# Kernel tuning notes

Measured on AMD Instinct MI355X. Metric: run time of the kernel, lower is better.

## Reference

```python
import jax, jax.numpy as jnp
import numpy as np

N_NODES = 100000
N_EDGES = 3200000
D = 16
L = 3


def setup_inputs() -> dict:
    key = jax.random.key(0)
    ks = jax.random.split(key, 7)
    scale = 1.0 / np.sqrt(D)
    x = jax.random.normal(ks[0], (N_NODES, D), dtype=jnp.float32)
    edge_index = jax.random.randint(ks[1], (2, N_EDGES), 0, N_NODES, dtype=jnp.int64)
    Wl = jax.random.normal(ks[2], (L, D, D), dtype=jnp.float32) * scale
    bl = jax.random.normal(ks[3], (L, D), dtype=jnp.float32) * scale
    Wr = jax.random.normal(ks[4], (L, D, D), dtype=jnp.float32) * scale
    Wlin = jax.random.normal(ks[5], (L, D, D), dtype=jnp.float32) * scale
    blin = jax.random.normal(ks[6], (L, D), dtype=jnp.float32) * scale
    return {"x": x, "edge_index": edge_index, "Wl": Wl, "bl": bl,
            "Wr": Wr, "Wlin": Wlin, "blin": blin}


def reference(x, edge_index, Wl, bl, Wr, Wlin, blin):
    src = edge_index[0]
    dst = edge_index[1]
    n = x.shape[0]
    # in-degree for mean aggregation (PyG SAGEConv aggr='mean')
    deg = jax.ops.segment_sum(jnp.ones((src.shape[0],), dtype=x.dtype), dst,
                              num_segments=n)
    denom = jnp.maximum(deg, 1.0)[:, None]  # nodes with no in-edges -> 0 agg
    for i in range(Wl.shape[0]):
        # gather source features, scatter-mean onto targets
        agg = jax.ops.segment_sum(x[src], dst, num_segments=n) / denom
        conv = agg @ Wl[i].T + bl[i] + x @ Wr[i].T  # SAGEConv: lin_l(agg)+lin_r(x)
        x = conv + x @ Wlin[i].T + blin[i]          # + Linear residual
    return x
```

## Files before the change

kernel.cpp:

```cpp
#include <hip/hip_runtime.h>

#define N_NODES 100000
#define N_EDGES 3200000
#define D 16
#define L 3

#define TILE 64
#define NB ((N_NODES + TILE - 1) / TILE)
#define CAP 3072
#define NBLK 500
#define SEG (N_EDGES / NBLK)
#define BINT 1024

__device__ __forceinline__ unsigned packbf(float a, float b) {
    unsigned ua = __float_as_uint(a); ua += 0x7FFFu + ((ua >> 16) & 1u);
    unsigned ub = __float_as_uint(b); ub += 0x7FFFu + ((ub >> 16) & 1u);
    return (ua >> 16) | (ub & 0xFFFF0000u);
}
#define BLO(u) __uint_as_float((u) << 16)
#define BHI(u) __uint_as_float((u) & 0xFFFF0000u)

__global__ void cvt_kernel(const float* __restrict__ x, unsigned* __restrict__ xbf, int n4) {
    int t = blockIdx.x * blockDim.x + threadIdx.x;
    if (t >= n4) return;
    float4 v = *(const float4*)(x + (size_t)t * 4);
    uint2 o; o.x = packbf(v.x, v.y); o.y = packbf(v.z, v.w);
    *(uint2*)(xbf + (size_t)t * 2) = o;
}

__global__ void bin_scatter(const int* __restrict__ src, const int* __restrict__ dst,
                            int* __restrict__ cursor, unsigned* __restrict__ ebuf, int E) {
    __shared__ int lcnt[NB];
    __shared__ int lbase[NB];
    for (int i = threadIdx.x; i < NB; i += BINT) lcnt[i] = 0;
    __syncthreads();
    int b0 = blockIdx.x * SEG, b1 = min(E, b0 + SEG);
    for (int e = b0 + threadIdx.x * 4; e < b1; e += BINT * 4) {
        int4 d4 = *(const int4*)(dst + e);
        atomicAdd(&lcnt[d4.x >> 6], 1);
        atomicAdd(&lcnt[d4.y >> 6], 1);
        atomicAdd(&lcnt[d4.z >> 6], 1);
        atomicAdd(&lcnt[d4.w >> 6], 1);
    }
    __syncthreads();
    for (int i = threadIdx.x; i < NB; i += BINT) {
        int v = lcnt[i];
        lbase[i] = v ? (i * CAP + atomicAdd(&cursor[i], v)) : 0;
    }
    __syncthreads();
    for (int i = threadIdx.x; i < NB; i += BINT) lcnt[i] = 0;
    __syncthreads();
    for (int e = b0 + threadIdx.x * 4; e < b1; e += BINT * 4) {
        int4 d4 = *(const int4*)(dst + e);
        int4 s4 = *(const int4*)(src + e);
        int b_, pos;
        b_ = d4.x >> 6; pos = lbase[b_] + atomicAdd(&lcnt[b_], 1);
        ebuf[pos] = ((unsigned)(d4.x & 63) << 17) | (unsigned)s4.x;
        b_ = d4.y >> 6; pos = lbase[b_] + atomicAdd(&lcnt[b_], 1);
        ebuf[pos] = ((unsigned)(d4.y & 63) << 17) | (unsigned)s4.y;
        b_ = d4.z >> 6; pos = lbase[b_] + atomicAdd(&lcnt[b_], 1);
        ebuf[pos] = ((unsigned)(d4.z & 63) << 17) | (unsigned)s4.z;
        b_ = d4.w >> 6; pos = lbase[b_] + atomicAdd(&lcnt[b_], 1);
        ebuf[pos] = ((unsigned)(d4.w & 63) << 17) | (unsigned)s4.w;
    }
}

__device__ __forceinline__ void agg_xform(
    const float* __restrict__ xin, const unsigned* __restrict__ xbf,
    const unsigned* se2, const int* lofs,
    const float* sWl, const float* sWc, const float* sbc,
    float* __restrict__ xout, unsigned* __restrict__ xbf_out,
    int emit_bf, int b, int N, int tid) {
    int n_loc = tid >> 2;
    int q = tid & 3;
    int n = b * TILE + n_loc;
    if (n >= N) return;

    int s0 = lofs[n_loc];
    int s1 = lofs[n_loc + 1];
    int deg = s1 - s0;

    float a0 = 0.f, a1 = 0.f, a2 = 0.f, a3 = 0.f;
    float c0 = 0.f, c1 = 0.f, c2 = 0.f, c3 = 0.f;
    int i = s0;
    for (; i + 8 <= s1; i += 8) {
        uint2 g[8];
        #pragma unroll
        for (int j = 0; j < 8; j++) {
            unsigned p = se2[i + j] & 0x1FFFF;
            g[j] = *(const uint2*)(xbf + (size_t)p * 8 + q * 2);
        }
        #pragma unroll
        for (int j = 0; j < 8; j += 2) {
            a0 += BLO(g[j].x); a1 += BHI(g[j].x); a2 += BLO(g[j].y); a3 += BHI(g[j].y);
            c0 += BLO(g[j + 1].x); c1 += BHI(g[j + 1].x); c2 += BLO(g[j + 1].y); c3 += BHI(g[j + 1].y);
        }
    }
    for (; i < s1; i++) {
        unsigned p = se2[i] & 0x1FFFF;
        uint2 g = *(const uint2*)(xbf + (size_t)p * 8 + q * 2);
        a0 += BLO(g.x); a1 += BHI(g.x); a2 += BLO(g.y); a3 += BHI(g.y);
    }
    a0 += c0; a1 += c1; a2 += c2; a3 += c3;

    float inv = 1.0f / fmaxf((float)deg, 1.0f);
    float a[4] = { a0 * inv, a1 * inv, a2 * inv, a3 * inv };
    float4 xq = *(const float4*)(xin + (size_t)n * D + q * 4);
    float xv[4] = { xq.x, xq.y, xq.z, xq.w };

    float o[4];
    #pragma unroll
    for (int j = 0; j < D; j++) {
        float p = 0.f;
        #pragma unroll
        for (int k = 0; k < 4; k++) {
            int kk = q * 4 + k;
            p += a[k] * sWl[j * D + kk] + xv[k] * sWc[j * D + kk];
        }
        p += __shfl_xor(p, 1, 4);
        p += __shfl_xor(p, 2, 4);
        if ((j >> 2) == q) o[j & 3] = p + sbc[j];
    }
    *(float4*)(xout + (size_t)n * D + q * 4) = make_float4(o[0], o[1], o[2], o[3]);
    if (emit_bf) {
        uint2 ob; ob.x = packbf(o[0], o[1]); ob.y = packbf(o[2], o[3]);
        *(uint2*)(xbf_out + (size_t)n * 8 + q * 2) = ob;
    }
}

__global__ void layer0_kernel(const float* __restrict__ xin, const unsigned* __restrict__ xbf,
                              unsigned* __restrict__ ebuf, const int* __restrict__ cnt,
                              int* __restrict__ node_start,
                              const float* __restrict__ Wl, const float* __restrict__ bl,
                              const float* __restrict__ Wr, const float* __restrict__ Wlin,
                              const float* __restrict__ blin,
                              float* __restrict__ xout, unsigned* __restrict__ xbf_out, int N) {
    __shared__ unsigned se[CAP];
    __shared__ unsigned se2[CAP];
    __shared__ int lcnt[TILE];
    __shared__ int lofs[TILE + 1];
    __shared__ float sWl[D * D];
    __shared__ float sWc[D * D];
    __shared__ float sbc[D];

    int tid = threadIdx.x;
    int b = blockIdx.x;
    int base = b * CAP;
    int nE = min(cnt[b], CAP);

    if (tid < D * D) { sWl[tid] = Wl[tid]; sWc[tid] = Wr[tid] + Wlin[tid]; }
    if (tid < D) sbc[tid] = bl[tid] + blin[tid];
    if (tid < TILE) lcnt[tid] = 0;
    __syncthreads();
    for (int i = tid; i < nE; i += 256) {
        unsigned p = ebuf[base + i];
        se[i] = p;
        atomicAdd(&lcnt[p >> 17], 1);
    }
    __syncthreads();
    if (tid < TILE) {
        int v = lcnt[tid];
        int s = v;
        #pragma unroll
        for (int d_ = 1; d_ < TILE; d_ <<= 1) {
            int t = __shfl_up(s, d_, TILE);
            if (tid >= d_) s += t;
        }
        int excl = s - v;
        lofs[tid] = excl;
        lcnt[tid] = excl;
        node_start[b * TILE + tid] = excl;
        if (tid == TILE - 1) lofs[TILE] = s;
    }
    __syncthreads();
    for (int i = tid; i < nE; i += 256) {
        unsigned p = se[i];
        int pos = atomicAdd(&lcnt[p >> 17], 1);
        se2[pos] = p;
    }
    __syncthreads();
    for (int i = tid; i < nE; i += 256)
        ebuf[base + i] = se2[i];

    agg_xform(xin, xbf, se2, lofs, sWl, sWc, sbc, xout, xbf_out, 1, b, N, tid);
}

__global__ void layerN_kernel(const float* __restrict__ xin, const unsigned* __restrict__ xbf,
                              const unsigned* __restrict__ ebuf, const int* __restrict__ cnt,
                              const int* __restrict__ node_start,
                              const float* __restrict__ Wl, const float* __restrict__ bl,
                              const float* __restrict__ Wr, const float* __restrict__ Wlin,
                              const float* __restrict__ blin,
                              float* __restrict__ xout, unsigned* __restrict__ xbf_out,
                              int emit_bf, int N) {
    __shared__ unsigned se2[CAP];
    __shared__ int lofs[TILE + 1];
    __shared__ float sWl[D * D];
    __shared__ float sWc[D * D];
    __shared__ float sbc[D];

    int tid = threadIdx.x;
    int b = blockIdx.x;
    int base = b * CAP;
    int nE = min(cnt[b], CAP);

    if (tid < D * D) { sWl[tid] = Wl[tid]; sWc[tid] = Wr[tid] + Wlin[tid]; }
    if (tid < D) sbc[tid] = bl[tid] + blin[tid];
    if (tid < TILE) lofs[tid] = node_start[b * TILE + tid];
    if (tid == 0) lofs[TILE] = nE;
    for (int i = tid; i < nE; i += 256) se2[i] = ebuf[base + i];
    __syncthreads();

    agg_xform(xin, xbf, se2, lofs, sWl, sWc, sbc, xout, xbf_out, emit_bf, b, N, tid);
}

extern "C" void kernel_launch(void* const* d_in, const int* in_sizes, int n_in,
                              void* d_out, int out_size, void* d_ws, size_t ws_size,
                              hipStream_t stream) {
    const float* x    = (const float*)d_in[0];
    const int*   ei   = (const int*)d_in[1];
    const float* Wl   = (const float*)d_in[2];
    const float* bl   = (const float*)d_in[3];
    const float* Wr   = (const float*)d_in[4];
    const float* Wlin = (const float*)d_in[5];
    const float* blin = (const float*)d_in[6];
    float* out = (float*)d_out;

    const int* src = ei;
    const int* dst = ei + N_EDGES;

    char* w = (char*)d_ws;
    unsigned* ebuf   = (unsigned*)w;  w += (size_t)NB * CAP * 4;
    float* bufA      = (float*)w;     w += (size_t)N_NODES * D * 4;
    float* bufB      = (float*)w;     w += (size_t)N_NODES * D * 4;
    unsigned* xbf0   = (unsigned*)w;  w += (size_t)N_NODES * 8 * 4;
    unsigned* xbf1   = (unsigned*)w;  w += (size_t)N_NODES * 8 * 4;
    int*   cursor    = (int*)w;       w += (size_t)NB * 4;
    int*   node_start= (int*)w;       w += (size_t)NB * TILE * 4;

    hipMemsetAsync(cursor, 0, (size_t)NB * 4, stream);
    cvt_kernel<<<(N_NODES * D / 4 + 255) / 256, 256, 0, stream>>>(x, xbf0, N_NODES * D / 4);
    bin_scatter<<<NBLK, BINT, 0, stream>>>(src, dst, cursor, ebuf, N_EDGES);

    layer0_kernel<<<NB, 256, 0, stream>>>(
        x, xbf0, ebuf, cursor, node_start,
        Wl, bl, Wr, Wlin, blin, bufA, xbf1, N_NODES);
    layerN_kernel<<<NB, 256, 0, stream>>>(
        bufA, xbf1, ebuf, cursor, node_start,
        Wl + D * D, bl + D, Wr + D * D, Wlin + D * D, blin + D, bufB, xbf0, 1, N_NODES);
    layerN_kernel<<<NB, 256, 0, stream>>>(
        bufB, xbf0, ebuf, cursor, node_start,
        Wl + 2 * D * D, bl + 2 * D, Wr + 2 * D * D, Wlin + 2 * D * D, blin + 2 * D,
        out, xbf1, 0, N_NODES);
}
```

Baseline: 217.1 us.

## Double node tile and sort nodes by degree within each tile

Doubles the per-block node tile to 128 nodes (512 threads, larger edge capacity) and computes a per-tile permutation that orders nodes by descending in-degree. The permutation is saved to global memory and reused by later layers, so the four lanes of a node and neighbouring nodes in a wavefront have similar edge counts. This targets load imbalance and divergence inside wavefronts during the gather loop. The cost is an O(TILE^2) rank computation in layer 0, a multi-step shared-memory scan with many barriers, and more shared memory per block, which can lower occupancy.

Measured after the change: 215.8 us. Within noise of the previous version (-0.6%).

```diff
diff --git a/kernel.cpp b/kernel.cpp
--- a/kernel.cpp
+++ b/kernel.cpp
@@ -5,12 +5,13 @@
 #define D 16
 #define L 3
 
-#define TILE 64
+#define TILE 128
 #define NB ((N_NODES + TILE - 1) / TILE)
-#define CAP 3072
+#define CAP 4608
 #define NBLK 500
 #define SEG (N_EDGES / NBLK)
 #define BINT 1024
+#define LT 512
 
 __device__ __forceinline__ unsigned packbf(float a, float b) {
     unsigned ua = __float_as_uint(a); ua += 0x7FFFu + ((ua >> 16) & 1u);
@@ -37,10 +38,10 @@
     int b0 = blockIdx.x * SEG, b1 = min(E, b0 + SEG);
     for (int e = b0 + threadIdx.x * 4; e < b1; e += BINT * 4) {
         int4 d4 = *(const int4*)(dst + e);
-        atomicAdd(&lcnt[d4.x >> 6], 1);
-        atomicAdd(&lcnt[d4.y >> 6], 1);
-        atomicAdd(&lcnt[d4.z >> 6], 1);
-        atomicAdd(&lcnt[d4.w >> 6], 1);
+        atomicAdd(&lcnt[d4.x >> 7], 1);
+        atomicAdd(&lcnt[d4.y >> 7], 1);
+        atomicAdd(&lcnt[d4.z >> 7], 1);
+        atomicAdd(&lcnt[d4.w >> 7], 1);
     }
     __syncthreads();
     for (int i = threadIdx.x; i < NB; i += BINT) {
@@ -54,25 +55,23 @@
         int4 d4 = *(const int4*)(dst + e);
         int4 s4 = *(const int4*)(src + e);
         int b_, pos;
-        b_ = d4.x >> 6; pos = lbase[b_] + atomicAdd(&lcnt[b_], 1);
-        ebuf[pos] = ((unsigned)(d4.x & 63) << 17) | (unsigned)s4.x;
-        b_ = d4.y >> 6; pos = lbase[b_] + atomicAdd(&lcnt[b_], 1);
-        ebuf[pos] = ((unsigned)(d4.y & 63) << 17) | (unsigned)s4.y;
-        b_ = d4.z >> 6; pos = lbase[b_] + atomicAdd(&lcnt[b_], 1);
-        ebuf[pos] = ((unsigned)(d4.z & 63) << 17) | (unsigned)s4.z;
-        b_ = d4.w >> 6; pos = lbase[b_] + atomicAdd(&lcnt[b_], 1);
-        ebuf[pos] = ((unsigned)(d4.w & 63) << 17) | (unsigned)s4.w;
+        b_ = d4.x >> 7; pos = lbase[b_] + atomicAdd(&lcnt[b_], 1);
+        ebuf[pos] = ((unsigned)(d4.x & 127) << 17) | (unsigned)s4.x;
+        b_ = d4.y >> 7; pos = lbase[b_] + atomicAdd(&lcnt[b_], 1);
+        ebuf[pos] = ((unsigned)(d4.y & 127) << 17) | (unsigned)s4.y;
+        b_ = d4.z >> 7; pos = lbase[b_] + atomicAdd(&lcnt[b_], 1);
+        ebuf[pos] = ((unsigned)(d4.z & 127) << 17) | (unsigned)s4.z;
+        b_ = d4.w >> 7; pos = lbase[b_] + atomicAdd(&lcnt[b_], 1);
+        ebuf[pos] = ((unsigned)(d4.w & 127) << 17) | (unsigned)s4.w;
     }
 }
 
 __device__ __forceinline__ void agg_xform(
     const float* __restrict__ xin, const unsigned* __restrict__ xbf,
-    const unsigned* se2, const int* lofs,
+    const unsigned* se2, const int* lofs, int n_loc,
     const float* sWl, const float* sWc, const float* sbc,
     float* __restrict__ xout, unsigned* __restrict__ xbf_out,
-    int emit_bf, int b, int N, int tid) {
-    int n_loc = tid >> 2;
-    int q = tid & 3;
+    int emit_bf, int b, int N, int q) {
     int n = b * TILE + n_loc;
     if (n >= N) return;
 
@@ -130,7 +129,7 @@
 
 __global__ void layer0_kernel(const float* __restrict__ xin, const unsigned* __restrict__ xbf,
                               unsigned* __restrict__ ebuf, const int* __restrict__ cnt,
-                              int* __restrict__ node_start,
+                              int* __restrict__ node_start, int* __restrict__ gperm,
                               const float* __restrict__ Wl, const float* __restrict__ bl,
                               const float* __restrict__ Wr, const float* __restrict__ Wlin,
                               const float* __restrict__ blin,
@@ -138,7 +137,10 @@
     __shared__ unsigned se[CAP];
     __shared__ unsigned se2[CAP];
     __shared__ int lcnt[TILE];
+    __shared__ int sscan[TILE];
     __shared__ int lofs[TILE + 1];
+    __shared__ int sdeg[TILE];
+    __shared__ int perm[TILE];
     __shared__ float sWl[D * D];
     __shared__ float sWc[D * D];
     __shared__ float sbc[D];
@@ -152,42 +154,55 @@
     if (tid < D) sbc[tid] = bl[tid] + blin[tid];
     if (tid < TILE) lcnt[tid] = 0;
     __syncthreads();
-    for (int i = tid; i < nE; i += 256) {
+    for (int i = tid; i < nE; i += LT) {
         unsigned p = ebuf[base + i];
         se[i] = p;
         atomicAdd(&lcnt[p >> 17], 1);
     }
     __syncthreads();
+    if (tid < TILE) sscan[tid] = lcnt[tid];
+    __syncthreads();
+    for (int off = 1; off < TILE; off <<= 1) {
+        int t = (tid < TILE && tid >= off) ? sscan[tid - off] : 0;
+        __syncthreads();
+        if (tid < TILE) sscan[tid] += t;
+        __syncthreads();
+    }
     if (tid < TILE) {
-        int v = lcnt[tid];
-        int s = v;
-        #pragma unroll
-        for (int d_ = 1; d_ < TILE; d_ <<= 1) {
-            int t = __shfl_up(s, d_, TILE);
-            if (tid >= d_) s += t;
-        }
-        int excl = s - v;
+        int excl = sscan[tid] - lcnt[tid];
         lofs[tid] = excl;
         lcnt[tid] = excl;
+        sdeg[tid] = sscan[tid] - excl;
         node_start[b * TILE + tid] = excl;
-        if (tid == TILE - 1) lofs[TILE] = s;
-    }
-    __syncthreads();
-    for (int i = tid; i < nE; i += 256) {
+        if (tid == TILE - 1) lofs[TILE] = sscan[tid];
+    }
+    __syncthreads();
+    if (tid < TILE) {
+        int dm = sdeg[tid];
+        int r = 0;
+        for (int j = 0; j < TILE; j++) {
+            int dj = sdeg[j];
+            r += (dj > dm) || (dj == dm && j < tid);
+        }
+        perm[r] = tid;
+        gperm[b * TILE + r] = tid;
+    }
+    for (int i = tid; i < nE; i += LT) {
         unsigned p = se[i];
         int pos = atomicAdd(&lcnt[p >> 17], 1);
         se2[pos] = p;
     }
     __syncthreads();
-    for (int i = tid; i < nE; i += 256)
+    for (int i = tid; i < nE; i += LT)
         ebuf[base + i] = se2[i];
 
-    agg_xform(xin, xbf, se2, lofs, sWl, sWc, sbc, xout, xbf_out, 1, b, N, tid);
+    agg_xform(xin, xbf, se2, lofs, perm[tid >> 2], sWl, sWc, sbc,
+              xout, xbf_out, 1, b, N, tid & 3);
 }
 
 __global__ void layerN_kernel(const float* __restrict__ xin, const unsigned* __restrict__ xbf,
                               const unsigned* __restrict__ ebuf, const int* __restrict__ cnt,
-                              const int* __restrict__ node_start,
+                              const int* __restrict__ node_start, const int* __restrict__ gperm,
                               const float* __restrict__ Wl, const float* __restrict__ bl,
                               const float* __restrict__ Wr, const float* __restrict__ Wlin,
                               const float* __restrict__ blin,
@@ -208,10 +223,12 @@
     if (tid < D) sbc[tid] = bl[tid] + blin[tid];
     if (tid < TILE) lofs[tid] = node_start[b * TILE + tid];
     if (tid == 0) lofs[TILE] = nE;
-    for (int i = tid; i < nE; i += 256) se2[i] = ebuf[base + i];
-    __syncthreads();
-
-    agg_xform(xin, xbf, se2, lofs, sWl, sWc, sbc, xout, xbf_out, emit_bf, b, N, tid);
+    for (int i = tid; i < nE; i += LT) se2[i] = ebuf[base + i];
+    int n_loc = gperm[b * TILE + (tid >> 2)];
+    __syncthreads();
+
+    agg_xform(xin, xbf, se2, lofs, n_loc, sWl, sWc, sbc,
+              xout, xbf_out, emit_bf, b, N, tid & 3);
 }
 
 extern "C" void kernel_launch(void* const* d_in, const int* in_sizes, int n_in,
@@ -237,19 +254,20 @@
     unsigned* xbf1   = (unsigned*)w;  w += (size_t)N_NODES * 8 * 4;
     int*   cursor    = (int*)w;       w += (size_t)NB * 4;
     int*   node_start= (int*)w;       w += (size_t)NB * TILE * 4;
+    int*   gperm     = (int*)w;       w += (size_t)NB * TILE * 4;
 
     hipMemsetAsync(cursor, 0, (size_t)NB * 4, stream);
     cvt_kernel<<<(N_NODES * D / 4 + 255) / 256, 256, 0, stream>>>(x, xbf0, N_NODES * D / 4);
     bin_scatter<<<NBLK, BINT, 0, stream>>>(src, dst, cursor, ebuf, N_EDGES);
 
-    layer0_kernel<<<NB, 256, 0, stream>>>(
-        x, xbf0, ebuf, cursor, node_start,
+    layer0_kernel<<<NB, LT, 0, stream>>>(
+        x, xbf0, ebuf, cursor, node_start, gperm,
         Wl, bl, Wr, Wlin, blin, bufA, xbf1, N_NODES);
-    layerN_kernel<<<NB, 256, 0, stream>>>(
-        bufA, xbf1, ebuf, cursor, node_start,
+    layerN_kernel<<<NB, LT, 0, stream>>>(
+        bufA, xbf1, ebuf, cursor, node_start, gperm,
         Wl + D * D, bl + D, Wr + D * D, Wlin + D * D, blin + D, bufB, xbf0, 1, N_NODES);
-    layerN_kernel<<<NB, 256, 0, stream>>>(
-        bufB, xbf0, ebuf, cursor, node_start,
+    layerN_kernel<<<NB, LT, 0, stream>>>(
+        bufB, xbf0, ebuf, cursor, node_start, gperm,
         Wl + 2 * D * D, bl + 2 * D, Wr + 2 * D * D, Wlin + 2 * D * D, blin + 2 * D,
         out, xbf1, 0, N_NODES);
 }
```
